# Kernel tuning notes

Measured on AMD Instinct MI355X. Metric: run time of the kernel, lower is better.

Reference implementation:

```python
import jax, jax.numpy as jnp
import numpy as np

B, T1, S, M = 64, 129, 128, 32   # batch, time-major dim, seq_len, num_series
U = 256                           # SkipGRUUnits
SKIP = 4                          # skip
HW = 128                          # highway window (== S by shape constraints)


def _skip_lstm(x_seq, kernel, rkernel, kernel2, bias, bias2, s0, units, skip):
    """Run the bespoke skip-LSTM cell over time. x_seq: (B, T, D) -> (B, T, U)."""
    Bx = x_seq.shape[0]
    # precompute input projections for all timesteps: (B, T, 4U)
    xW = jnp.einsum('btd,du->btu', x_seq, kernel) + bias
    # recurrent kernel viewed per-gate: Rk[:, g, :] == rkernel[:, g*U:(g+1)*U]
    Rk = rkernel.reshape(units, 4, units)

    def step(carry, x_t):
        h_tm1, c_tm1, prev_h = carry            # (B,4U), (B,U), (B,U*skip)
        x_i, x_f, x_c, x_o = jnp.split(x_t, 4, axis=1)
        hg = h_tm1.reshape(Bx, 4, units)        # gate-specific previous state
        r = jnp.einsum('bgu,ugv->bgv', hg, Rk)  # (B,4,U)
        i = jax.nn.sigmoid(x_i + r[:, 0])
        f = jax.nn.sigmoid(x_f + r[:, 1])
        c = f * c_tm1 + i * jnp.tanh(x_c + r[:, 2])
        o = jax.nn.sigmoid(x_o + r[:, 3])
        h = o * jnp.tanh(c)
        h_skip = jax.nn.sigmoid(prev_h[:, :units] @ kernel2 + bias2)
        h = s0 * h + (1.0 - s0) * h_skip
        new_h_tm1 = jnp.concatenate([i, f, c, o], axis=1)
        new_prev = jnp.concatenate([prev_h[:, units:], h], axis=1)
        return (new_h_tm1, c, new_prev), h

    init = (jnp.zeros((Bx, 4 * units), x_seq.dtype),
            jnp.zeros((Bx, units), x_seq.dtype),
            jnp.zeros((Bx, units * skip), x_seq.dtype))
    _, hs = jax.lax.scan(step, init, jnp.swapaxes(xW, 0, 1))  # (T,B,U)
    return jnp.swapaxes(hs, 0, 1)


def setup_inputs() -> dict:
    key = jax.random.key(0)
    ks = jax.random.split(key, 10)
    g = lambda k, shape, s=0.05: (jax.random.normal(k, shape, jnp.float32) * s)
    return {
        'X': jax.random.normal(ks[0], (B, T1, S, M), jnp.float32),
        'enc_kernel': g(ks[1], (M, 4 * U)),
        'enc_rkernel': g(ks[2], (U, 4 * U)),
        'enc_kernel2': g(ks[3], (U, U)),
        'enc_bias': jnp.zeros((4 * U,), jnp.float32),
        'enc_bias2': jnp.zeros((U,), jnp.float32),
        'enc_s0': jnp.float32(0.5),
        'dec_kernel': g(ks[4], (U, 4 * U)),
        'dec_rkernel': g(ks[5], (U, 4 * U)),
        'dec_kernel2': g(ks[6], (U, U)),
        'dec_bias': jnp.zeros((4 * U,), jnp.float32),
        'dec_bias2': jnp.zeros((U,), jnp.float32),
        'dec_s0': jnp.float32(0.5),
        'dense_w': g(ks[7], (S * U, S * M), 0.01),
        'dense_b': jnp.zeros((S * M,), jnp.float32),
        'final_w': g(ks[8], (HW,), 0.05),
        'final_b': jnp.zeros((), jnp.float32),
    }


def reference(X, enc_kernel, enc_rkernel, enc_kernel2, enc_bias, enc_bias2, enc_s0,
              dec_kernel, dec_rkernel, dec_kernel2, dec_bias, dec_bias2, dec_s0,
              dense_w, dense_b, final_w, final_b):
    X1 = X[:, 0]        # (B, S, M) encoder input
    X2 = X[:, 1:]       # (B, T1-1, S, M) highway inputs
    SE = _skip_lstm(X1, enc_kernel, enc_rkernel, enc_kernel2, enc_bias, enc_bias2, enc_s0, U, SKIP)
    SD = _skip_lstm(SE, dec_kernel, dec_rkernel, dec_kernel2, dec_bias, dec_bias2, dec_s0, U, SKIP)
    RD = SD.reshape(X.shape[0], S * U)
    Y = (RD @ dense_w + dense_b).reshape(-1, S, M)  # (B, S, M)
    # highway: PreARTrans takes last HW steps, shared final Linear(S->1) over time axis
    Z2 = jnp.einsum('bism,s->bim', X2[:, :, -HW:, :], final_w) + final_b  # (B, T1-1, M)
    return Y + Z2
```

## Files before the change

### kernel.cpp

```cpp
#include <hip/hip_runtime.h>
#include <hip/hip_fp16.h>


typedef _Float16 h8 __attribute__((ext_vector_type(8)));
typedef float f4v __attribute__((ext_vector_type(4)));

__device__ __forceinline__ float sigmoidf_(float x) {
    return 1.0f / (1.0f + __expf(-x));
}
__device__ __forceinline__ float tanhf_(float x) {
    float xc = fminf(fmaxf(x, -15.f), 15.f);
    float e = __expf(2.f * xc);
    return (e - 1.f) / (e + 1.f);
}
__device__ __forceinline__ unsigned pkh(float lo, float hi) {
    __half2 h = __halves2half2(__float2half(lo), __float2half(hi));
    return *reinterpret_cast<unsigned*>(&h);
}
__device__ __forceinline__ float2 uph(unsigned u) {
    __half2 h = *reinterpret_cast<__half2*>(&u);
    return __half22float2(h);
}

__global__ __launch_bounds__(256) void packall(
    const float* __restrict__ e_rk, const float* __restrict__ d_rk,
    const float* __restrict__ d_k,  const float* __restrict__ e_k,
    const float* __restrict__ e_k2, const float* __restrict__ d_k2,
    float4* __restrict__ rk4e, float4* __restrict__ rk4d,
    float4* __restrict__ dk4,  float4* __restrict__ ek4,
    unsigned* __restrict__ kh2e, unsigned* __restrict__ kh2d,
    unsigned* __restrict__ flags)
{
    const int bx = blockIdx.x, v = threadIdx.x;
    if (bx < 800) {
        const float* src; float4* dst; int row;
        if (bx < 256)      { src = e_rk; dst = rk4e; row = bx; }
        else if (bx < 512) { src = d_rk; dst = rk4d; row = bx - 256; }
        else if (bx < 768) { src = d_k;  dst = dk4;  row = bx - 512; }
        else               { src = e_k;  dst = ek4;  row = bx - 768; }
        const float* s = src + (size_t)row * 1024;
        dst[row * 256 + v] = make_float4(s[v], s[256 + v], s[512 + v], s[768 + v]);
    } else if (bx < 928) {
        const int u2 = bx - 800;
        kh2e[u2 * 256 + v] = pkh(e_k2[(2 * u2) * 256 + v], e_k2[(2 * u2 + 1) * 256 + v]);
        kh2d[u2 * 256 + v] = pkh(d_k2[(2 * u2) * 256 + v], d_k2[(2 * u2 + 1) * 256 + v]);
    } else {
        flags[v] = 0u;
    }
}

__global__ __launch_bounds__(256) void xw_gemm_enc(
    const float*  __restrict__ X,
    const float4* __restrict__ ek4,
    const float*  __restrict__ bias,
    float4* __restrict__ xWp)
{
    const int v = threadIdx.x;
    const int r0 = blockIdx.x * 16;
    __shared__ float se[16][32];

    #pragma unroll
    for (int p = 0; p < 2; ++p) {
        int idx = p * 256 + v;
        int rr = idx >> 5, d = idx & 31;
        int R = r0 + rr, b = R >> 7, t = R & 127;
        se[rr][d] = X[((size_t)b * 129 * 128 + t) * 32 + d];
    }
    __syncthreads();

    float4 bv = make_float4(bias[v], bias[256 + v], bias[512 + v], bias[768 + v]);
    float4 acc[16];
    #pragma unroll
    for (int rr = 0; rr < 16; ++rr) acc[rr] = bv;

    #pragma unroll
    for (int u = 0; u < 32; ++u) {
        float4 w = ek4[u * 256 + v];
        #pragma unroll
        for (int rr = 0; rr < 16; ++rr) {
            float s = se[rr][u];
            acc[rr].x += s * w.x; acc[rr].y += s * w.y;
            acc[rr].z += s * w.z; acc[rr].w += s * w.w;
        }
    }
    #pragma unroll
    for (int rr = 0; rr < 16; ++rr)
        xWp[(size_t)(r0 + rr) * 256 + v] = acc[rr];
}

__global__ __launch_bounds__(512) void xw_gemm_dec(
    const float*  __restrict__ SE,
    const float4* __restrict__ dk4,
    const float*  __restrict__ bias,
    float4* __restrict__ xWp)
{
    const int tid = threadIdx.x;
    const int v = tid & 255;
    const int hh = tid >> 8;
    const int rbase = blockIdx.x * 32;
    __shared__ float se[32][256];

    for (int i = tid; i < 8192; i += 512) {
        int rr = i >> 8, c = i & 255;
        se[rr][c] = SE[(size_t)(rbase + rr) * 256 + c];
    }
    __syncthreads();

    float4 bv = make_float4(bias[v], bias[256 + v], bias[512 + v], bias[768 + v]);
    float4 acc[16];
    #pragma unroll
    for (int rr = 0; rr < 16; ++rr) acc[rr] = bv;

    #pragma unroll 8
    for (int u = 0; u < 256; ++u) {
        float4 w = dk4[u * 256 + v];
        #pragma unroll
        for (int rr = 0; rr < 16; ++rr) {
            float s = se[hh * 16 + rr][u];
            acc[rr].x += s * w.x; acc[rr].y += s * w.y;
            acc[rr].z += s * w.z; acc[rr].w += s * w.w;
        }
    }
    #pragma unroll
    for (int rr = 0; rr < 16; ++rr)
        xWp[(size_t)(rbase + hh * 16 + rr) * 256 + v] = acc[rr];
}

__global__ __launch_bounds__(1024, 4) void rec9(
    const float4*   __restrict__ xW,
    const float4*   __restrict__ rk4,
    const unsigned* __restrict__ kh2,
    const float*    __restrict__ bias2,
    const float*    __restrict__ s0p,
    float* __restrict__ out,
    _Float16* __restrict__ outh,
    float* __restrict__ EX,
    unsigned* __restrict__ flags,
    unsigned fbase)
{
    const int b     = blockIdx.x & 63;
    const int slice = blockIdx.x >> 6;
    const int voff  = slice * 64;
    const int tid   = threadIdx.x;
    const int us    = tid >> 6;
    const int vl    = tid & 63;
    const int v     = voff + vl;

    __shared__ float4 wres[128][64];
    __shared__ float4 pA[16][64];
    __shared__ float  pS[16][64];
    __shared__ float4 h4[256];
    __shared__ float  pq[4][256];

    for (int i = tid; i < 8192; i += 1024) {
        int r = i >> 6, vv = i & 63;
        int cc = r >> 3, j = r & 7;
        wres[r][vv] = rk4[(cc * 16 + j) * 256 + voff + vv];
    }
    float4 wreg[8];
    unsigned kreg[8];
    {
        const float4*   wp = rk4 + (us * 16 + 8) * 256 + v;
        const unsigned* kp = kh2 + (us * 8) * 256 + v;
        #pragma unroll
        for (int j = 0; j < 8; ++j) wreg[j] = wp[j * 256];
        #pragma unroll
        for (int j = 0; j < 8; ++j) kreg[j] = kp[j * 256];
    }
    if (tid < 256) {
        h4[tid] = make_float4(0.f, 0.f, 0.f, 0.f);
        pq[0][tid] = 0.f; pq[1][tid] = 0.f; pq[2][tid] = 0.f; pq[3][tid] = 0.f;
    }
    float cst = 0.f;
    const float s0 = s0p[0];
    const float b2 = bias2[voff + vl];
    unsigned* mflag = flags + b * 4 + slice;
    __syncthreads();

    for (int t = 0; t < 128; ++t) {
        float4 xa = make_float4(0.f, 0.f, 0.f, 0.f);
        if (tid < 64) xa = xW[((size_t)b * 128 + t) * 256 + voff + tid];
        if (t > 0 && tid < 3) {
            int ps = tid + (tid >= slice ? 1 : 0);
            const unsigned* pf = flags + b * 4 + ps;
            while (__hip_atomic_load(pf, __ATOMIC_RELAXED, __HIP_MEMORY_SCOPE_AGENT) < fbase + (unsigned)t)
                __builtin_amdgcn_s_sleep(2);
        }
        __syncthreads();
        if (t > 0) {
            const int sp = (t + 1) & 1;
            if (tid < 480) {
                int pi = tid / 160;
                int j  = tid - pi * 160;
                int ps = pi + (pi >= slice ? 1 : 0);
                const unsigned long long* src = (const unsigned long long*)
                    (EX + (((size_t)sp * 64 + b) * 4 + ps) * 320);
                unsigned long long d = __hip_atomic_load(src + j, __ATOMIC_RELAXED, __HIP_MEMORY_SCOPE_AGENT);
                if (j < 128) {
                    reinterpret_cast<unsigned long long*>(&h4[ps * 64])[j] = d;
                } else {
                    int k = j - 128;
                    union { unsigned long long u; float f[2]; } cv; cv.u = d;
                    pq[(t + 3) & 3][ps * 64 + 2 * k]     = cv.f[0];
                    pq[(t + 3) & 3][ps * 64 + 2 * k + 1] = cv.f[1];
                }
            }
        }
        __syncthreads();

        float ai = 0.f, af = 0.f, acg = 0.f, ao = 0.f, as = 0.f;
        const int slot = t & 3;
        #pragma unroll
        for (int j = 0; j < 8; ++j) {
            float4 w = wres[us * 8 + j][vl];
            float4 g = h4[us * 16 + j];
            ai += g.x * w.x; af += g.y * w.y; acg += g.z * w.z; ao += g.w * w.w;
        }
        #pragma unroll
        for (int j = 0; j < 8; ++j) {
            float4 w = wreg[j];
            float4 g = h4[us * 16 + 8 + j];
            ai += g.x * w.x; af += g.y * w.y; acg += g.z * w.z; ao += g.w * w.w;
        }
        #pragma unroll
        for (int j = 0; j < 8; ++j) {
            float2 kk = uph(kreg[j]);
            as += pq[slot][us * 16 + 2 * j] * kk.x + pq[slot][us * 16 + 2 * j + 1] * kk.y;
        }
        pA[us][vl] = make_float4(ai, af, acg, ao);
        pS[us][vl] = as;
        __syncthreads();

        if (tid < 64) {
            float4 A = pA[0][vl];
            float  S = pS[0][vl];
            #pragma unroll
            for (int cc = 1; cc < 16; ++cc) {
                float4 q = pA[cc][vl];
                A.x += q.x; A.y += q.y; A.z += q.z; A.w += q.w;
                S += pS[cc][vl];
            }
            float gi = sigmoidf_(xa.x + A.x);
            float gf = sigmoidf_(xa.y + A.y);
            float cb = tanhf_(xa.z + A.z);
            cst = gf * cst + gi * cb;
            float go = sigmoidf_(xa.w + A.w);
            float hh = go * tanhf_(cst);
            float hs = sigmoidf_(S + b2);
            float hf = s0 * hh + (1.f - s0) * hs;
            h4[voff + vl] = make_float4(gi, gf, cst, go);
            pq[slot][voff + vl] = hf;
            if (outh) outh[((size_t)b * 128 + t) * 256 + voff + vl] = (_Float16)hf;
            else      out [((size_t)b * 128 + t) * 256 + voff + vl] = hf;
            float* dst = EX + (((size_t)(t & 1) * 64 + b) * 4 + slice) * 320;
            union { float4 f4; unsigned long long u[2]; } gv;
            gv.f4 = make_float4(gi, gf, cst, go);
            __hip_atomic_store((unsigned long long*)dst + 2 * vl,     gv.u[0], __ATOMIC_RELAXED, __HIP_MEMORY_SCOPE_AGENT);
            __hip_atomic_store((unsigned long long*)dst + 2 * vl + 1, gv.u[1], __ATOMIC_RELAXED, __HIP_MEMORY_SCOPE_AGENT);
            __hip_atomic_store(dst + 256 + vl, hf, __ATOMIC_RELAXED, __HIP_MEMORY_SCOPE_AGENT);
        }
        __syncthreads();
        if (tid == 0)
            __hip_atomic_store(mflag, fbase + (unsigned)(t + 1), __ATOMIC_RELAXED, __HIP_MEMORY_SCOPE_AGENT);
    }
}

__global__ __launch_bounds__(256, 4) void mfma_dense(
    const _Float16* __restrict__ SDh,
    const float*    __restrict__ dw,
    float* __restrict__ P)
{
    const int nb  = blockIdx.x & 63;
    const int kc  = blockIdx.x >> 6;
    const int n0  = nb * 64;
    const int tid = threadIdx.x;
    const int w   = tid >> 6;
    const int l   = tid & 63;
    const int ar  = l & 15;
    const int ko8 = (l >> 4) * 8;
    const int rq  = tid >> 4;
    const int nq  = tid & 15;

    __shared__ unsigned Bt[64][36];

    f4v acc[4] = {{0.f,0.f,0.f,0.f},{0.f,0.f,0.f,0.f},{0.f,0.f,0.f,0.f},{0.f,0.f,0.f,0.f}};

    for (int kk = 0; kk < 32; ++kk) {
        const int kg = kc * 2048 + kk * 64;
        {
            const float* base = dw + (size_t)(kg + rq * 4) * 4096 + n0 + nq * 4;
            float4 r0 = *reinterpret_cast<const float4*>(base);
            float4 r1 = *reinterpret_cast<const float4*>(base + 4096);
            float4 r2 = *reinterpret_cast<const float4*>(base + 2 * 4096);
            float4 r3 = *reinterpret_cast<const float4*>(base + 3 * 4096);
            const int k2a = rq * 2, k2b = rq * 2 + 1;
            Bt[nq * 4 + 0][k2a] = pkh(r0.x, r1.x);
            Bt[nq * 4 + 1][k2a] = pkh(r0.y, r1.y);
            Bt[nq * 4 + 2][k2a] = pkh(r0.z, r1.z);
            Bt[nq * 4 + 3][k2a] = pkh(r0.w, r1.w);
            Bt[nq * 4 + 0][k2b] = pkh(r2.x, r3.x);
            Bt[nq * 4 + 1][k2b] = pkh(r2.y, r3.y);
            Bt[nq * 4 + 2][k2b] = pkh(r2.z, r3.z);
            Bt[nq * 4 + 3][k2b] = pkh(r2.w, r3.w);
        }
        __syncthreads();
        #pragma unroll
        for (int hs = 0; hs < 2; ++hs) {
            const int kw = kg + hs * 32;
            h8 bf = *reinterpret_cast<const h8*>(
                      reinterpret_cast<const _Float16*>(&Bt[16 * w + ar][0]) + hs * 32 + ko8);
            #pragma unroll
            for (int mt = 0; mt < 4; ++mt) {
                h8 af = *reinterpret_cast<const h8*>(
                          SDh + (size_t)(mt * 16 + ar) * 32768 + kw + ko8);
                acc[mt] = __builtin_amdgcn_mfma_f32_16x16x32_f16(af, bf, acc[mt], 0, 0, 0);
            }
        }
        __syncthreads();
    }
    #pragma unroll
    for (int mt = 0; mt < 4; ++mt) {
        #pragma unroll
        for (int r = 0; r < 4; ++r) {
            P[(size_t)(kc * 64 + mt * 16 + (l >> 4) * 4 + r) * 4096 + n0 + 16 * w + ar] = acc[mt][r];
        }
    }
}

__global__ __launch_bounds__(256) void reduce_z2(
    const float* __restrict__ P,
    const float* __restrict__ db,
    const float* __restrict__ X,
    const float* __restrict__ fw,
    const float* __restrict__ fbp,
    float* __restrict__ out)
{
    const int o4 = blockIdx.x * 256 + threadIdx.x;
    const int b  = o4 >> 10;
    const int j4 = o4 & 1023;
    const int j0 = j4 * 4;
    const int i  = j0 >> 5;
    const int m  = j0 & 31;

    float4 acc = *reinterpret_cast<const float4*>(db + j0);
    #pragma unroll
    for (int kc = 0; kc < 16; ++kc) {
        float4 p = *reinterpret_cast<const float4*>(P + (size_t)(kc * 64 + b) * 4096 + j0);
        acc.x += p.x; acc.y += p.y; acc.z += p.z; acc.w += p.w;
    }

    const float* xp = X + ((size_t)(b * 129 + 1 + i) * 128) * 32 + m;
    #pragma unroll 8
    for (int s = 0; s < 128; ++s) {
        float4 xv = *reinterpret_cast<const float4*>(xp + (size_t)s * 32);
        float w = fw[s];
        acc.x += w * xv.x; acc.y += w * xv.y; acc.z += w * xv.z; acc.w += w * xv.w;
    }
    const float fb = fbp[0];
    acc.x += fb; acc.y += fb; acc.z += fb; acc.w += fb;
    *reinterpret_cast<float4*>(out + (size_t)o4 * 4) = acc;
}

extern "C" void kernel_launch(void* const* d_in, const int* in_sizes, int n_in,
                              void* d_out, int out_size, void* d_ws, size_t ws_size,
                              hipStream_t stream) {
    const float* X    = (const float*)d_in[0];
    const float* e_k  = (const float*)d_in[1];
    const float* e_rk = (const float*)d_in[2];
    const float* e_k2 = (const float*)d_in[3];
    const float* e_b  = (const float*)d_in[4];
    const float* e_b2 = (const float*)d_in[5];
    const float* e_s0 = (const float*)d_in[6];
    const float* d_k  = (const float*)d_in[7];
    const float* d_rk = (const float*)d_in[8];
    const float* d_k2 = (const float*)d_in[9];
    const float* d_b  = (const float*)d_in[10];
    const float* d_b2 = (const float*)d_in[11];
    const float* d_s0 = (const float*)d_in[12];
    const float* dw   = (const float*)d_in[13];
    const float* db   = (const float*)d_in[14];
    const float* fw   = (const float*)d_in[15];
    const float* fb   = (const float*)d_in[16];

    float* ws = (float*)d_ws;
    float4*   rk4e  = (float4*)(ws);
    float4*   rk4d  = (float4*)(ws + 262144);
    float4*   dk4   = (float4*)(ws + 524288);
    float4*   ek4   = (float4*)(ws + 786432);
    unsigned* kh2e  = (unsigned*)(ws + 819200);
    unsigned* kh2d  = (unsigned*)(ws + 851968);
    float*    EX    = ws + 884736;
    unsigned* flags = (unsigned*)(ws + 1212416);
    float*    xW    = ws + 1310720;
    float*    SE    = ws + 9699328;
    _Float16* SDh   = (_Float16*)(ws + 11796480);

    float* P = xW;

    hipLaunchKernelGGL(packall, dim3(929), dim3(256), 0, stream,
                       e_rk, d_rk, d_k, e_k, e_k2, d_k2,
                       rk4e, rk4d, dk4, ek4, kh2e, kh2d, flags);
    hipLaunchKernelGGL(xw_gemm_enc, dim3(512), dim3(256), 0, stream,
                       X, ek4, e_b, (float4*)xW);
    hipLaunchKernelGGL(rec9, dim3(256), dim3(1024), 0, stream,
                       (const float4*)xW, rk4e, kh2e, e_b2, e_s0, SE, (_Float16*)nullptr,
                       EX, flags, 0u);
    hipLaunchKernelGGL(xw_gemm_dec, dim3(256), dim3(512), 0, stream,
                       SE, dk4, d_b, (float4*)xW);
    hipLaunchKernelGGL(rec9, dim3(256), dim3(1024), 0, stream,
                       (const float4*)xW, rk4d, kh2d, d_b2, d_s0, (float*)nullptr, SDh,
                       EX, flags, 128u);
    hipLaunchKernelGGL(mfma_dense, dim3(1024), dim3(256), 0, stream, SDh, dw, P);
    hipLaunchKernelGGL(reduce_z2, dim3(256), dim3(256), 0, stream,
                       P, db, X, fw, fb, (float*)d_out);
}
```

Before: 1.055 ms.

## Fuse encoder recurrence, decoder input GEMM and decoder recurrence into one kernel

Merges the two recurrent-cell launches and the decoder input-projection GEMM into one persistent kernel, with one block per (batch, 64-unit slice). After the encoder phase, each block waits on the per-batch flags of its sibling slices. It then computes its own slice of the decoder input projection from the encoder output, reloads the decoder weights, and runs the decoder recurrence. This removes two kernel launches and boundaries and keeps the data for each batch local. The trade-off is that the decoder GEMM now runs on only 256 big blocks with 16-row tiles, and re-reads its weight slice eight times, so it may use the GPU less efficiently than the standalone GEMM did.

After: 1.237 ms. +17.2%, slower.

```diff
diff --git a/kernel.cpp b/kernel.cpp
--- a/kernel.cpp
+++ b/kernel.cpp
@@ -88,55 +88,18 @@
         xWp[(size_t)(r0 + rr) * 256 + v] = acc[rr];
 }
 
-__global__ __launch_bounds__(512) void xw_gemm_dec(
-    const float*  __restrict__ SE,
-    const float4* __restrict__ dk4,
-    const float*  __restrict__ bias,
-    float4* __restrict__ xWp)
-{
-    const int tid = threadIdx.x;
-    const int v = tid & 255;
-    const int hh = tid >> 8;
-    const int rbase = blockIdx.x * 32;
-    __shared__ float se[32][256];
-
-    for (int i = tid; i < 8192; i += 512) {
-        int rr = i >> 8, c = i & 255;
-        se[rr][c] = SE[(size_t)(rbase + rr) * 256 + c];
-    }
-    __syncthreads();
-
-    float4 bv = make_float4(bias[v], bias[256 + v], bias[512 + v], bias[768 + v]);
-    float4 acc[16];
-    #pragma unroll
-    for (int rr = 0; rr < 16; ++rr) acc[rr] = bv;
-
-    #pragma unroll 8
-    for (int u = 0; u < 256; ++u) {
-        float4 w = dk4[u * 256 + v];
-        #pragma unroll
-        for (int rr = 0; rr < 16; ++rr) {
-            float s = se[hh * 16 + rr][u];
-            acc[rr].x += s * w.x; acc[rr].y += s * w.y;
-            acc[rr].z += s * w.z; acc[rr].w += s * w.w;
-        }
-    }
-    #pragma unroll
-    for (int rr = 0; rr < 16; ++rr)
-        xWp[(size_t)(rbase + hh * 16 + rr) * 256 + v] = acc[rr];
-}
-
-__global__ __launch_bounds__(1024, 4) void rec9(
-    const float4*   __restrict__ xW,
-    const float4*   __restrict__ rk4,
-    const unsigned* __restrict__ kh2,
-    const float*    __restrict__ bias2,
-    const float*    __restrict__ s0p,
-    float* __restrict__ out,
-    _Float16* __restrict__ outh,
-    float* __restrict__ EX,
-    unsigned* __restrict__ flags,
-    unsigned fbase)
+__global__ __launch_bounds__(1024, 4) void rec_fused(
+    const float4*   __restrict__ xWe,
+    float4*         __restrict__ xWd,
+    const float4*   __restrict__ rk4e, const unsigned* __restrict__ kh2e,
+    const float*    __restrict__ e_b2, const float* __restrict__ e_s0,
+    const float4*   __restrict__ rk4d, const unsigned* __restrict__ kh2d,
+    const float*    __restrict__ d_b2, const float* __restrict__ d_s0,
+    const float4*   __restrict__ dk4,  const float* __restrict__ d_b,
+    float*          __restrict__ SE,
+    _Float16*       __restrict__ SDh,
+    float*          __restrict__ EX,
+    unsigned*       __restrict__ flags)
 {
     const int b     = blockIdx.x & 63;
     const int slice = blockIdx.x >> 6;
@@ -152,117 +115,164 @@
     __shared__ float4 h4[256];
     __shared__ float  pq[4][256];
 
-    for (int i = tid; i < 8192; i += 1024) {
-        int r = i >> 6, vv = i & 63;
-        int cc = r >> 3, j = r & 7;
-        wres[r][vv] = rk4[(cc * 16 + j) * 256 + voff + vv];
-    }
     float4 wreg[8];
     unsigned kreg[8];
-    {
+    float cst;
+    float s0, b2;
+    unsigned* mflag = flags + b * 4 + slice;
+
+    auto loadw = [&](const float4* rk4, const unsigned* kh2) {
+        for (int i = tid; i < 8192; i += 1024) {
+            int r = i >> 6, vv = i & 63;
+            int cc = r >> 3, j = r & 7;
+            wres[r][vv] = rk4[(cc * 16 + j) * 256 + voff + vv];
+        }
         const float4*   wp = rk4 + (us * 16 + 8) * 256 + v;
         const unsigned* kp = kh2 + (us * 8) * 256 + v;
         #pragma unroll
         for (int j = 0; j < 8; ++j) wreg[j] = wp[j * 256];
         #pragma unroll
         for (int j = 0; j < 8; ++j) kreg[j] = kp[j * 256];
-    }
-    if (tid < 256) {
-        h4[tid] = make_float4(0.f, 0.f, 0.f, 0.f);
-        pq[0][tid] = 0.f; pq[1][tid] = 0.f; pq[2][tid] = 0.f; pq[3][tid] = 0.f;
-    }
-    float cst = 0.f;
-    const float s0 = s0p[0];
-    const float b2 = bias2[voff + vl];
-    unsigned* mflag = flags + b * 4 + slice;
+        if (tid < 256) {
+            h4[tid] = make_float4(0.f, 0.f, 0.f, 0.f);
+            pq[0][tid] = 0.f; pq[1][tid] = 0.f; pq[2][tid] = 0.f; pq[3][tid] = 0.f;
+        }
+        cst = 0.f;
+    };
+
+    auto phase = [&](unsigned fbase, const float4* xaP, int mode) {
+        for (int t = 0; t < 128; ++t) {
+            float4 xa = make_float4(0.f, 0.f, 0.f, 0.f);
+            if (tid < 64) xa = xaP[((size_t)b * 128 + t) * 256 + voff + tid];
+            if (t > 0 && tid < 3) {
+                int ps = tid + (tid >= slice ? 1 : 0);
+                const unsigned* pf = flags + b * 4 + ps;
+                while (__hip_atomic_load(pf, __ATOMIC_RELAXED, __HIP_MEMORY_SCOPE_AGENT) < fbase + (unsigned)t)
+                    __builtin_amdgcn_s_sleep(2);
+            }
+            __syncthreads();
+            if (t > 0) {
+                const int sp = (t + 1) & 1;
+                if (tid < 480) {
+                    int pi = tid / 160;
+                    int j  = tid - pi * 160;
+                    int ps = pi + (pi >= slice ? 1 : 0);
+                    const unsigned long long* src = (const unsigned long long*)
+                        (EX + (((size_t)sp * 64 + b) * 4 + ps) * 320);
+                    unsigned long long d = __hip_atomic_load(src + j, __ATOMIC_RELAXED, __HIP_MEMORY_SCOPE_AGENT);
+                    if (j < 128) {
+                        reinterpret_cast<unsigned long long*>(&h4[ps * 64])[j] = d;
+                    } else {
+                        int k = j - 128;
+                        union { unsigned long long u; float f[2]; } cv; cv.u = d;
+                        pq[(t + 3) & 3][ps * 64 + 2 * k]     = cv.f[0];
+                        pq[(t + 3) & 3][ps * 64 + 2 * k + 1] = cv.f[1];
+                    }
+                }
+            }
+            __syncthreads();
+
+            float ai = 0.f, af = 0.f, acg = 0.f, ao = 0.f, as = 0.f;
+            const int slot = t & 3;
+            #pragma unroll
+            for (int j = 0; j < 8; ++j) {
+                float4 w = wres[us * 8 + j][vl];
+                float4 g = h4[us * 16 + j];
+                ai += g.x * w.x; af += g.y * w.y; acg += g.z * w.z; ao += g.w * w.w;
+            }
+            #pragma unroll
+            for (int j = 0; j < 8; ++j) {
+                float4 w = wreg[j];
+                float4 g = h4[us * 16 + 8 + j];
+                ai += g.x * w.x; af += g.y * w.y; acg += g.z * w.z; ao += g.w * w.w;
+            }
+            #pragma unroll
+            for (int j = 0; j < 8; ++j) {
+                float2 kk = uph(kreg[j]);
+                as += pq[slot][us * 16 + 2 * j] * kk.x + pq[slot][us * 16 + 2 * j + 1] * kk.y;
+            }
+            pA[us][vl] = make_float4(ai, af, acg, ao);
+            pS[us][vl] = as;
+            __syncthreads();
+
+            if (tid < 64) {
+                float4 A = pA[0][vl];
+                float  S = pS[0][vl];
+                #pragma unroll
+                for (int cc = 1; cc < 16; ++cc) {
+                    float4 q = pA[cc][vl];
+                    A.x += q.x; A.y += q.y; A.z += q.z; A.w += q.w;
+                    S += pS[cc][vl];
+                }
+                float gi = sigmoidf_(xa.x + A.x);
+                float gf = sigmoidf_(xa.y + A.y);
+                float cb = tanhf_(xa.z + A.z);
+                cst = gf * cst + gi * cb;
+                float go = sigmoidf_(xa.w + A.w);
+                float hh = go * tanhf_(cst);
+                float hs = sigmoidf_(S + b2);
+                float hf = s0 * hh + (1.f - s0) * hs;
+                h4[voff + vl] = make_float4(gi, gf, cst, go);
+                pq[slot][voff + vl] = hf;
+                const size_t oi = ((size_t)b * 128 + t) * 256 + voff + vl;
+                if (mode == 0)
+                    __hip_atomic_store(SE + oi, hf, __ATOMIC_RELAXED, __HIP_MEMORY_SCOPE_AGENT);
+                else
+                    SDh[oi] = (_Float16)hf;
+                float* dst = EX + (((size_t)(t & 1) * 64 + b) * 4 + slice) * 320;
+                union { float4 f4; unsigned long long u[2]; } gv;
+                gv.f4 = make_float4(gi, gf, cst, go);
+                __hip_atomic_store((unsigned long long*)dst + 2 * vl,     gv.u[0], __ATOMIC_RELAXED, __HIP_MEMORY_SCOPE_AGENT);
+                __hip_atomic_store((unsigned long long*)dst + 2 * vl + 1, gv.u[1], __ATOMIC_RELAXED, __HIP_MEMORY_SCOPE_AGENT);
+                __hip_atomic_store(dst + 256 + vl, hf, __ATOMIC_RELAXED, __HIP_MEMORY_SCOPE_AGENT);
+            }
+            __syncthreads();
+            if (tid == 0)
+                __hip_atomic_store(mflag, fbase + (unsigned)(t + 1), __ATOMIC_RELAXED, __HIP_MEMORY_SCOPE_AGENT);
+        }
+    };
+
+    loadw(rk4e, kh2e);
+    s0 = e_s0[0]; b2 = e_b2[v];
     __syncthreads();
-
-    for (int t = 0; t < 128; ++t) {
-        float4 xa = make_float4(0.f, 0.f, 0.f, 0.f);
-        if (tid < 64) xa = xW[((size_t)b * 128 + t) * 256 + voff + tid];
-        if (t > 0 && tid < 3) {
-            int ps = tid + (tid >= slice ? 1 : 0);
-            const unsigned* pf = flags + b * 4 + ps;
-            while (__hip_atomic_load(pf, __ATOMIC_RELAXED, __HIP_MEMORY_SCOPE_AGENT) < fbase + (unsigned)t)
-                __builtin_amdgcn_s_sleep(2);
-        }
-        __syncthreads();
-        if (t > 0) {
-            const int sp = (t + 1) & 1;
-            if (tid < 480) {
-                int pi = tid / 160;
-                int j  = tid - pi * 160;
-                int ps = pi + (pi >= slice ? 1 : 0);
-                const unsigned long long* src = (const unsigned long long*)
-                    (EX + (((size_t)sp * 64 + b) * 4 + ps) * 320);
-                unsigned long long d = __hip_atomic_load(src + j, __ATOMIC_RELAXED, __HIP_MEMORY_SCOPE_AGENT);
-                if (j < 128) {
-                    reinterpret_cast<unsigned long long*>(&h4[ps * 64])[j] = d;
-                } else {
-                    int k = j - 128;
-                    union { unsigned long long u; float f[2]; } cv; cv.u = d;
-                    pq[(t + 3) & 3][ps * 64 + 2 * k]     = cv.f[0];
-                    pq[(t + 3) & 3][ps * 64 + 2 * k + 1] = cv.f[1];
-                }
-            }
-        }
-        __syncthreads();
-
-        float ai = 0.f, af = 0.f, acg = 0.f, ao = 0.f, as = 0.f;
-        const int slot = t & 3;
-        #pragma unroll
-        for (int j = 0; j < 8; ++j) {
-            float4 w = wres[us * 8 + j][vl];
-            float4 g = h4[us * 16 + j];
-            ai += g.x * w.x; af += g.y * w.y; acg += g.z * w.z; ao += g.w * w.w;
-        }
-        #pragma unroll
-        for (int j = 0; j < 8; ++j) {
-            float4 w = wreg[j];
-            float4 g = h4[us * 16 + 8 + j];
-            ai += g.x * w.x; af += g.y * w.y; acg += g.z * w.z; ao += g.w * w.w;
-        }
-        #pragma unroll
-        for (int j = 0; j < 8; ++j) {
-            float2 kk = uph(kreg[j]);
-            as += pq[slot][us * 16 + 2 * j] * kk.x + pq[slot][us * 16 + 2 * j + 1] * kk.y;
-        }
-        pA[us][vl] = make_float4(ai, af, acg, ao);
-        pS[us][vl] = as;
-        __syncthreads();
-
-        if (tid < 64) {
-            float4 A = pA[0][vl];
-            float  S = pS[0][vl];
-            #pragma unroll
-            for (int cc = 1; cc < 16; ++cc) {
-                float4 q = pA[cc][vl];
-                A.x += q.x; A.y += q.y; A.z += q.z; A.w += q.w;
-                S += pS[cc][vl];
-            }
-            float gi = sigmoidf_(xa.x + A.x);
-            float gf = sigmoidf_(xa.y + A.y);
-            float cb = tanhf_(xa.z + A.z);
-            cst = gf * cst + gi * cb;
-            float go = sigmoidf_(xa.w + A.w);
-            float hh = go * tanhf_(cst);
-            float hs = sigmoidf_(S + b2);
-            float hf = s0 * hh + (1.f - s0) * hs;
-            h4[voff + vl] = make_float4(gi, gf, cst, go);
-            pq[slot][voff + vl] = hf;
-            if (outh) outh[((size_t)b * 128 + t) * 256 + voff + vl] = (_Float16)hf;
-            else      out [((size_t)b * 128 + t) * 256 + voff + vl] = hf;
-            float* dst = EX + (((size_t)(t & 1) * 64 + b) * 4 + slice) * 320;
-            union { float4 f4; unsigned long long u[2]; } gv;
-            gv.f4 = make_float4(gi, gf, cst, go);
-            __hip_atomic_store((unsigned long long*)dst + 2 * vl,     gv.u[0], __ATOMIC_RELAXED, __HIP_MEMORY_SCOPE_AGENT);
-            __hip_atomic_store((unsigned long long*)dst + 2 * vl + 1, gv.u[1], __ATOMIC_RELAXED, __HIP_MEMORY_SCOPE_AGENT);
-            __hip_atomic_store(dst + 256 + vl, hf, __ATOMIC_RELAXED, __HIP_MEMORY_SCOPE_AGENT);
-        }
-        __syncthreads();
-        if (tid == 0)
-            __hip_atomic_store(mflag, fbase + (unsigned)(t + 1), __ATOMIC_RELAXED, __HIP_MEMORY_SCOPE_AGENT);
-    }
+    phase(0u, xWe, 0);
+
+    if (tid < 3) {
+        int ps = tid + (tid >= slice ? 1 : 0);
+        const unsigned* pf = flags + b * 4 + ps;
+        while (__hip_atomic_load(pf, __ATOMIC_RELAXED, __HIP_MEMORY_SCOPE_AGENT) < 128u)
+            __builtin_amdgcn_s_sleep(2);
+    }
+    __syncthreads();
+
+    {
+        float4 bv = make_float4(d_b[v], d_b[256 + v], d_b[512 + v], d_b[768 + v]);
+        float* seL = reinterpret_cast<float*>(&pA[0][0]);
+        const int tt = tid >> 6;
+        for (int tile = 0; tile < 8; ++tile) {
+            for (int i = tid; i < 4096; i += 1024) {
+                int r = i >> 8, u = i & 255;
+                seL[r * 256 + u] = __hip_atomic_load(
+                    SE + ((size_t)b * 128 + tile * 16 + r) * 256 + u,
+                    __ATOMIC_RELAXED, __HIP_MEMORY_SCOPE_AGENT);
+            }
+            __syncthreads();
+            float4 acc = bv;
+            #pragma unroll 8
+            for (int u = 0; u < 256; ++u) {
+                float s = seL[tt * 256 + u];
+                float4 w = dk4[u * 256 + v];
+                acc.x += s * w.x; acc.y += s * w.y; acc.z += s * w.z; acc.w += s * w.w;
+            }
+            xWd[((size_t)b * 128 + tile * 16 + tt) * 256 + v] = acc;
+            __syncthreads();
+        }
+    }
+
+    loadw(rk4d, kh2d);
+    s0 = d_s0[0]; b2 = d_b2[v];
+    __syncthreads();
+    phase(256u, (const float4*)xWd, 1);
 }
 
 __global__ __launch_bounds__(256, 4) void mfma_dense(
@@ -402,14 +412,12 @@
                        rk4e, rk4d, dk4, ek4, kh2e, kh2d, flags);
     hipLaunchKernelGGL(xw_gemm_enc, dim3(512), dim3(256), 0, stream,
                        X, ek4, e_b, (float4*)xW);
-    hipLaunchKernelGGL(rec9, dim3(256), dim3(1024), 0, stream,
-                       (const float4*)xW, rk4e, kh2e, e_b2, e_s0, SE, (_Float16*)nullptr,
-                       EX, flags, 0u);
-    hipLaunchKernelGGL(xw_gemm_dec, dim3(256), dim3(512), 0, stream,
-                       SE, dk4, d_b, (float4*)xW);
-    hipLaunchKernelGGL(rec9, dim3(256), dim3(1024), 0, stream,
-                       (const float4*)xW, rk4d, kh2d, d_b2, d_s0, (float*)nullptr, SDh,
-                       EX, flags, 128u);
+    hipLaunchKernelGGL(rec_fused, dim3(256), dim3(1024), 0, stream,
+                       (const float4*)xW, (float4*)xW,
+                       rk4e, kh2e, e_b2, e_s0,
+                       rk4d, kh2d, d_b2, d_s0,
+                       dk4, d_b,
+                       SE, SDh, EX, flags);
     hipLaunchKernelGGL(mfma_dense, dim3(1024), dim3(256), 0, stream, SDh, dw, P);
     hipLaunchKernelGGL(reduce_z2, dim3(256), dim3(256), 0, stream,
                        P, db, X, fw, fb, (float*)d_out);
```
